# Kernel tuning notes

Hardware: AMD Instinct MI355X
Metric: run time of the kernel (lower is better)

## Reference

```python
import jax, jax.numpy as jnp
import numpy as np

B, T, C = 4, 2048, 1024
H = 16
D = C // H  # head_dim = 64


def setup_inputs() -> dict:
    key = jax.random.key(0)
    k1, k2, k3 = jax.random.split(key, 3)
    x = jax.random.normal(k1, (B, T, C), dtype=jnp.float32)
    w_qkv = jax.random.normal(k2, (3 * C, C), dtype=jnp.float32) * (1.0 / np.sqrt(C))
    w_proj = jax.random.normal(k3, (C, C), dtype=jnp.float32) * (1.0 / np.sqrt(C))
    return {"x": x, "w_qkv": w_qkv, "w_proj": w_proj}


def reference(x, w_qkv, w_proj):
    Bx, Tx, Cx = x.shape
    qkv = jnp.einsum('btc,fc->btf', x, w_qkv)  # [B,T,3C]
    q, k, v = jnp.split(qkv, 3, axis=-1)
    # [B,H,T,D]
    q = q.reshape(Bx, Tx, H, D).transpose(0, 2, 1, 3)
    k = k.reshape(Bx, Tx, H, D).transpose(0, 2, 1, 3)
    v = v.reshape(Bx, Tx, H, D).transpose(0, 2, 1, 3)
    scale = 1.0 / np.sqrt(D)
    scores = jnp.einsum('bhqd,bhkd->bhqk', q, k) * scale
    causal = jnp.tril(jnp.ones((Tx, Tx), dtype=bool))
    scores = jnp.where(causal, scores, jnp.finfo(scores.dtype).min)
    attn = jax.nn.softmax(scores, axis=-1)
    out = jnp.einsum('bhqk,bhkd->bhqd', attn, v)  # [B,H,T,D]
    out = out.transpose(0, 2, 1, 3).reshape(Bx, Tx, Cx)
    return jnp.einsum('btc,oc->bto', out, w_proj)
```

## Files before the change

### kernel.cpp

```cpp
#include <hip/hip_runtime.h>
#include <hip/hip_bf16.h>
#include <stdint.h>

#define Bx 4
#define Tx 2048
#define Cx 1024
#define Hx 16
#define Dx 64
#define Mx (Bx*Tx)

typedef __bf16 bf16x8 __attribute__((ext_vector_type(8)));
typedef float f32x4 __attribute__((ext_vector_type(4)));
typedef unsigned short u16x8 __attribute__((ext_vector_type(8)));

__device__ __forceinline__ unsigned short f2bf(float f) {
  union { float f; unsigned u; } v; v.f = f;
  unsigned r = v.u + 0x7fffu + ((v.u >> 16) & 1u);
  return (unsigned short)(r >> 16);
}

__global__ void cvt_kernel(const float* __restrict__ in, unsigned short* __restrict__ out, int n) {
  int i = blockIdx.x * blockDim.x + threadIdx.x;
  int idx = i << 3;
  if (idx >= n) return;
  const float4* p = (const float4*)(in + idx);
  float4 a = p[0], b = p[1];
  u16x8 o;
  o[0] = f2bf(a.x); o[1] = f2bf(a.y); o[2] = f2bf(a.z); o[3] = f2bf(a.w);
  o[4] = f2bf(b.x); o[5] = f2bf(b.y); o[6] = f2bf(b.z); o[7] = f2bf(b.w);
  *(u16x8*)(out + idx) = o;
}

#define GLOAD_LDS16(g, l) \
  __builtin_amdgcn_global_load_lds((const __attribute__((address_space(1))) void*)(g), \
                                   (__attribute__((address_space(3))) void*)(l), 16, 0, 0)

template<int OUT_F32>
__global__ __launch_bounds__(256) void gemm_nt(const unsigned short* __restrict__ A,
                                               const unsigned short* __restrict__ Bm,
                                               void* __restrict__ Cv,
                                               int M, int N, int K)
{
  __shared__ unsigned short As[128 * 32];
  __shared__ unsigned short Bs[128 * 32];
  const int tid  = threadIdx.x;
  const int wave = tid >> 6, lane = tid & 63;
  const int l15 = lane & 15, l4 = lane >> 4;
  const int mBase = blockIdx.y << 7;
  const int nBase = blockIdx.x << 7;
  const int wm = wave >> 1, wn = wave & 1;

  const int srow  = (wave << 4) + (lane >> 2);
  const int skcol = (lane & 3) << 3;

  f32x4 acc[4][4];
  #pragma unroll
  for (int i = 0; i < 4; ++i)
    #pragma unroll
    for (int j = 0; j < 4; ++j) { acc[i][j][0] = 0.f; acc[i][j][1] = 0.f; acc[i][j][2] = 0.f; acc[i][j][3] = 0.f; }

  const unsigned short* aRow = A  + (size_t)(mBase + srow) * K + skcol;
  const unsigned short* bRow = Bm + (size_t)(nBase + srow) * K + skcol;
  unsigned short* aL0 = As + (wave << 9);
  unsigned short* bL0 = Bs + (wave << 9);

  for (int k0 = 0; k0 < K; k0 += 32) {
    GLOAD_LDS16(aRow + k0,                   aL0);
    GLOAD_LDS16(aRow + (size_t)64 * K + k0,  aL0 + 2048);
    GLOAD_LDS16(bRow + k0,                   bL0);
    GLOAD_LDS16(bRow + (size_t)64 * K + k0,  bL0 + 2048);
    __syncthreads();

    bf16x8 af[4], bfr[4];
    #pragma unroll
    for (int mi = 0; mi < 4; ++mi)
      af[mi] = *(const bf16x8*)&As[((wm << 6) + (mi << 4) + l15) * 32 + (l4 << 3)];
    #pragma unroll
    for (int nj = 0; nj < 4; ++nj)
      bfr[nj] = *(const bf16x8*)&Bs[((wn << 6) + (nj << 4) + l15) * 32 + (l4 << 3)];
    #pragma unroll
    for (int mi = 0; mi < 4; ++mi)
      #pragma unroll
      for (int nj = 0; nj < 4; ++nj)
        acc[mi][nj] = __builtin_amdgcn_mfma_f32_16x16x32_bf16(af[mi], bfr[nj], acc[mi][nj], 0, 0, 0);
    __syncthreads();
  }

  #pragma unroll
  for (int mi = 0; mi < 4; ++mi) {
    #pragma unroll
    for (int nj = 0; nj < 4; ++nj) {
      const int row = mBase + (wm << 6) + (mi << 4) + (l4 << 2);
      const int col = nBase + (wn << 6) + (nj << 4) + l15;
      #pragma unroll
      for (int r = 0; r < 4; ++r) {
        float v = acc[mi][nj][r];
        if (OUT_F32) ((float*)Cv)[(size_t)(row + r) * N + col] = v;
        else ((unsigned short*)Cv)[(size_t)(row + r) * N + col] = f2bf(v);
      }
    }
  }
}

__global__ void vtrans_kernel(const unsigned short* __restrict__ qkv, unsigned short* __restrict__ vt) {
  const int bh = blockIdx.y;
  const int b = bh >> 4, h = bh & 15;
  const int t0 = blockIdx.x << 6;
  __shared__ unsigned short tile[64][65];
  const int tid = threadIdx.x;
  const unsigned short* src = qkv + (size_t)b * Tx * 3072 + 2048 + h * 64;
  for (int e = tid; e < 4096; e += 256) {
    int r = e >> 6, c = e & 63;
    tile[c][r] = src[(size_t)(t0 + r) * 3072 + c];
  }
  __syncthreads();
  unsigned short* dst = vt + (size_t)bh * 64 * Tx + t0;
  for (int e = tid; e < 4096; e += 256) {
    int d = e >> 6, tt = e & 63;
    dst[(size_t)d * Tx + tt] = tile[d][tt];
  }
}

__device__ __forceinline__ void compute_half(
    const unsigned short* __restrict__ Ks, const unsigned short* __restrict__ Vs,
    unsigned short* __restrict__ Plw,
    bf16x8 aq0, bf16x8 aq1, float* m_run, float* rs, f32x4* oacc,
    int qrow0, int kv0, bool diag, int l15, int l4)
{
  const float SC = 0.125f * 1.44269504f;
  f32x4 s[4];
  #pragma unroll
  for (int nt = 0; nt < 4; ++nt) { s[nt][0]=0.f; s[nt][1]=0.f; s[nt][2]=0.f; s[nt][3]=0.f; }
  #pragma unroll
  for (int nt = 0; nt < 4; ++nt) {
    const int r = (nt << 4) + l15, sz = r & 7;
    bf16x8 bk0 = *(const bf16x8*)&Ks[r * 64 + ((l4 ^ sz) << 3)];
    bf16x8 bk1 = *(const bf16x8*)&Ks[r * 64 + (((l4 + 4) ^ sz) << 3)];
    s[nt] = __builtin_amdgcn_mfma_f32_16x16x32_bf16(aq0, bk0, s[nt], 0, 0, 0);
    s[nt] = __builtin_amdgcn_mfma_f32_16x16x32_bf16(aq1, bk1, s[nt], 0, 0, 0);
  }
  #pragma unroll
  for (int nt = 0; nt < 4; ++nt) {
    const int kv = kv0 + (nt << 4) + l15;
    #pragma unroll
    for (int r = 0; r < 4; ++r) {
      float val = s[nt][r] * SC;
      if (diag && kv > qrow0 + (l4 << 2) + r) val = -3.0e38f;
      s[nt][r] = val;
    }
  }
  float pm[4];
  #pragma unroll
  for (int r = 0; r < 4; ++r)
    pm[r] = fmaxf(fmaxf(s[0][r], s[1][r]), fmaxf(s[2][r], s[3][r]));
  int ok = (pm[0] <= m_run[0] + 8.f) & (pm[1] <= m_run[1] + 8.f)
         & (pm[2] <= m_run[2] + 8.f) & (pm[3] <= m_run[3] + 8.f);
  if (!__all(ok)) {
    #pragma unroll
    for (int off = 1; off < 16; off <<= 1)
      #pragma unroll
      for (int r = 0; r < 4; ++r) pm[r] = fmaxf(pm[r], __shfl_xor(pm[r], off));
    #pragma unroll
    for (int r = 0; r < 4; ++r) {
      float mnew = fmaxf(m_run[r], pm[r]);
      float corr = exp2f(m_run[r] - mnew);
      rs[r] *= corr;
      #pragma unroll
      for (int nt = 0; nt < 4; ++nt) oacc[nt][r] *= corr;
      m_run[r] = mnew;
    }
  }
  #pragma unroll
  for (int nt = 0; nt < 4; ++nt)
    #pragma unroll
    for (int r = 0; r < 4; ++r) {
      float p = exp2f(s[nt][r] - m_run[r]);
      s[nt][r] = p;
      rs[r] += p;
    }
  #pragma unroll
  for (int nt = 0; nt < 4; ++nt)
    #pragma unroll
    for (int r = 0; r < 4; ++r)
      Plw[((l4 << 2) + r) * 72 + (nt << 4) + l15] = f2bf(s[nt][r]);
  asm volatile("s_waitcnt lgkmcnt(0)" ::: "memory");
  __builtin_amdgcn_sched_barrier(0);
  bf16x8 ap0 = *(const bf16x8*)&Plw[l15 * 72 + (l4 << 3)];
  bf16x8 ap1 = *(const bf16x8*)&Plw[l15 * 72 + 32 + (l4 << 3)];
  #pragma unroll
  for (int nt = 0; nt < 4; ++nt) {
    const int r = (nt << 4) + l15, vz = r & 7;
    bf16x8 bv0 = *(const bf16x8*)&Vs[r * 64 + ((l4 ^ vz) << 3)];
    bf16x8 bv1 = *(const bf16x8*)&Vs[r * 64 + (((l4 + 4) ^ vz) << 3)];
    oacc[nt] = __builtin_amdgcn_mfma_f32_16x16x32_bf16(ap0, bv0, oacc[nt], 0, 0, 0);
    oacc[nt] = __builtin_amdgcn_mfma_f32_16x16x32_bf16(ap1, bv1, oacc[nt], 0, 0, 0);
  }
}

__global__ __launch_bounds__(256, 4) void attn_kernel(const unsigned short* __restrict__ qkv,
                                                      const unsigned short* __restrict__ vt,
                                                      unsigned short* __restrict__ aout)
{
  const int id = blockIdx.x;
  const int xcd = id & 7, sblk = id >> 3;
  const int xblk = sblk & 15;
  const int bh = (xcd << 3) + (sblk >> 4);
  const int b = bh >> 4, h = bh & 15;
  const int wave = threadIdx.x >> 6, lane = threadIdx.x & 63;
  const int l15 = lane & 15, l4 = lane >> 4;
  const int qi0 = (xblk << 2) + wave;

  const unsigned short* qp = qkv + (size_t)b * Tx * 3072 + h * 64;
  const unsigned short* kp = qp + 1024;
  const unsigned short* vp = vt + (size_t)bh * 64 * Tx;
  unsigned short* op = aout + (size_t)b * Tx * 1024 + h * 64;

  __shared__ unsigned short Ks[64 * 64];
  __shared__ unsigned short Vs[64 * 64];
  __shared__ unsigned short Pl[4][2][16 * 72];

  const int qiA = qi0, qiB = 127 - qi0;
  const int qrA = qiA << 4, qrB = qiB << 4;
  const int lastA = xblk, lastB = 31 - xblk;

  bf16x8 aqA0 = *(const bf16x8*)&qp[(size_t)(qrA + l15) * 3072 + (l4 << 3)];
  bf16x8 aqA1 = *(const bf16x8*)&qp[(size_t)(qrA + l15) * 3072 + 32 + (l4 << 3)];
  bf16x8 aqB0 = *(const bf16x8*)&qp[(size_t)(qrB + l15) * 3072 + (l4 << 3)];
  bf16x8 aqB1 = *(const bf16x8*)&qp[(size_t)(qrB + l15) * 3072 + 32 + (l4 << 3)];

  float mA[4], rsA[4], mB[4], rsB[4];
  f32x4 oA[4], oB[4];
  #pragma unroll
  for (int r = 0; r < 4; ++r) { mA[r]=0.f; rsA[r]=0.f; mB[r]=0.f; rsB[r]=0.f; }
  #pragma unroll
  for (int nt = 0; nt < 4; ++nt) {
    oA[nt][0]=0.f; oA[nt][1]=0.f; oA[nt][2]=0.f; oA[nt][3]=0.f;
    oB[nt][0]=0.f; oB[nt][1]=0.f; oB[nt][2]=0.f; oB[nt][3]=0.f;
  }

  const int srw = lane >> 3;
  const int sj  = (lane & 7) ^ srw;

  for (int kvt = 0; kvt <= lastB; ++kvt) {
    const int kv0 = kvt << 6;
    {
      const int c0 = wave << 1, c1 = c0 + 1;
      const int r0 = (c0 << 3) + srw, r1 = (c1 << 3) + srw;
      GLOAD_LDS16(kp + (size_t)(kv0 + r0) * 3072 + (sj << 3), Ks + (c0 << 9));
      GLOAD_LDS16(kp + (size_t)(kv0 + r1) * 3072 + (sj << 3), Ks + (c1 << 9));
      GLOAD_LDS16(vp + (size_t)r0 * 2048 + kv0 + (sj << 3),   Vs + (c0 << 9));
      GLOAD_LDS16(vp + (size_t)r1 * 2048 + kv0 + (sj << 3),   Vs + (c1 << 9));
    }
    __syncthreads();

    compute_half(Ks, Vs, Pl[wave][1], aqB0, aqB1, mB, rsB, oB, qrB, kv0, kvt == lastB, l15, l4);
    if (kvt <= lastA)
      compute_half(Ks, Vs, Pl[wave][0], aqA0, aqA1, mA, rsA, oA, qrA, kv0, kvt == lastA, l15, l4);

    __syncthreads();
  }

  #pragma unroll
  for (int off = 1; off < 16; off <<= 1)
    #pragma unroll
    for (int r = 0; r < 4; ++r) { rsA[r] += __shfl_xor(rsA[r], off); rsB[r] += __shfl_xor(rsB[r], off); }
  #pragma unroll
  for (int r = 0; r < 4; ++r) {
    const float invA = 1.0f / rsA[r], invB = 1.0f / rsB[r];
    #pragma unroll
    for (int nt = 0; nt < 4; ++nt) {
      op[(size_t)(qrA + (l4 << 2) + r) * 1024 + (nt << 4) + l15] = f2bf(oA[nt][r] * invA);
      op[(size_t)(qrB + (l4 << 2) + r) * 1024 + (nt << 4) + l15] = f2bf(oB[nt][r] * invB);
    }
  }
}

extern "C" void kernel_launch(void* const* d_in, const int* in_sizes, int n_in,
                              void* d_out, int out_size, void* d_ws, size_t ws_size,
                              hipStream_t stream) {
  const float* x     = (const float*)d_in[0];
  const float* wqkv  = (const float*)d_in[1];
  const float* wproj = (const float*)d_in[2];

  char* ws = (char*)d_ws;
  unsigned short* qkvb = (unsigned short*)(ws);
  unsigned short* vtb  = (unsigned short*)(ws + 50331648);
  unsigned short* xb   = (unsigned short*)(ws + 50331648 + 16777216);
  unsigned short* wqb  = (unsigned short*)(ws + 50331648 + 16777216 + 16777216);
  unsigned short* wpb  = (unsigned short*)(ws + 50331648 + 16777216 + 16777216 + 6291456);
  unsigned short* aob  = xb;

  cvt_kernel<<<4096, 256, 0, stream>>>(x,     xb,  Bx * Tx * Cx);
  cvt_kernel<<<1536, 256, 0, stream>>>(wqkv,  wqb, 3 * Cx * Cx);
  cvt_kernel<<<512,  256, 0, stream>>>(wproj, wpb, Cx * Cx);

  gemm_nt<0><<<dim3(24, 64), 256, 0, stream>>>(xb, wqb, qkvb, Mx, 3072, 1024);
  vtrans_kernel<<<dim3(32, 64), 256, 0, stream>>>(qkvb, vtb);
  attn_kernel<<<1024, 256, 0, stream>>>(qkvb, vtb, aob);
  gemm_nt<1><<<dim3(8, 64), 256, 0, stream>>>(aob, wpb, d_out, Mx, 1024, 1024);
}
```

Measured before the change: 309.5 us.

## Rewrite bf16 GEMMs with double-buffered LDS, 256x128 tiles, swizzle and XCD remap

Replaces the single-buffered 128x128x32 GEMM with a 512-thread kernel using 256x128 tiles, K-step 64 and double-buffered direct-to-LDS loads. The next tile's loads are issued before computing on the current one, waiting only with vmcnt. LDS chunks are XOR-swizzled to reduce bank conflicts. Block IDs are remapped across the 8 XCDs for L2 locality, and MFMA sections get raised wave priority. The aim is to hide global-load latency and raise MFMA utilisation in the QKV and projection GEMMs, at the cost of more LDS per block and lower occupancy.

```diff
diff --git a/kernel.cpp b/kernel.cpp
--- a/kernel.cpp
+++ b/kernel.cpp
@@ -36,58 +36,87 @@
                                    (__attribute__((address_space(3))) void*)(l), 16, 0, 0)
 
 template<int OUT_F32>
-__global__ __launch_bounds__(256) void gemm_nt(const unsigned short* __restrict__ A,
-                                               const unsigned short* __restrict__ Bm,
-                                               void* __restrict__ Cv,
-                                               int M, int N, int K)
+__global__ __launch_bounds__(512, 1) void gemm8p(const unsigned short* __restrict__ A,
+                                                 const unsigned short* __restrict__ Bm,
+                                                 void* __restrict__ Cv,
+                                                 int M, int N, int K)
 {
-  __shared__ unsigned short As[128 * 32];
-  __shared__ unsigned short Bs[128 * 32];
-  const int tid  = threadIdx.x;
+  __shared__ unsigned short As[2][256 * 64];
+  __shared__ unsigned short Bs[2][128 * 64];
+  const int tid = threadIdx.x;
   const int wave = tid >> 6, lane = tid & 63;
   const int l15 = lane & 15, l4 = lane >> 4;
-  const int mBase = blockIdx.y << 7;
-  const int nBase = blockIdx.x << 7;
   const int wm = wave >> 1, wn = wave & 1;
-
-  const int srow  = (wave << 4) + (lane >> 2);
-  const int skcol = (lane & 3) << 3;
+  const int NB = N >> 7;
+  const int cpx = (int)gridDim.x >> 3;
+  const int bid = (int)blockIdx.x;
+  const int swz = (bid & 7) * cpx + (bid >> 3);
+  const int bx = swz % NB, by = swz / NB;
+  const int mBase = by << 8, nBase = bx << 7;
+
+  const int srow   = tid >> 3;
+  const int schunk = (tid & 7) ^ (srow & 7);
+  const unsigned short* aSrc = A  + (size_t)(mBase + srow) * K + (schunk << 3);
+  const unsigned short* bSrc = Bm + (size_t)(nBase + srow) * K + (schunk << 3);
+  const int dstOff = wave << 9;
 
   f32x4 acc[4][4];
   #pragma unroll
   for (int i = 0; i < 4; ++i)
     #pragma unroll
-    for (int j = 0; j < 4; ++j) { acc[i][j][0] = 0.f; acc[i][j][1] = 0.f; acc[i][j][2] = 0.f; acc[i][j][3] = 0.f; }
-
-  const unsigned short* aRow = A  + (size_t)(mBase + srow) * K + skcol;
-  const unsigned short* bRow = Bm + (size_t)(nBase + srow) * K + skcol;
-  unsigned short* aL0 = As + (wave << 9);
-  unsigned short* bL0 = Bs + (wave << 9);
-
-  for (int k0 = 0; k0 < K; k0 += 32) {
-    GLOAD_LDS16(aRow + k0,                   aL0);
-    GLOAD_LDS16(aRow + (size_t)64 * K + k0,  aL0 + 2048);
-    GLOAD_LDS16(bRow + k0,                   bL0);
-    GLOAD_LDS16(bRow + (size_t)64 * K + k0,  bL0 + 2048);
-    __syncthreads();
-
-    bf16x8 af[4], bfr[4];
-    #pragma unroll
-    for (int mi = 0; mi < 4; ++mi)
-      af[mi] = *(const bf16x8*)&As[((wm << 6) + (mi << 4) + l15) * 32 + (l4 << 3)];
-    #pragma unroll
-    for (int nj = 0; nj < 4; ++nj)
-      bfr[nj] = *(const bf16x8*)&Bs[((wn << 6) + (nj << 4) + l15) * 32 + (l4 << 3)];
-    #pragma unroll
-    for (int mi = 0; mi < 4; ++mi)
+    for (int j = 0; j < 4; ++j) { acc[i][j][0]=0.f; acc[i][j][1]=0.f; acc[i][j][2]=0.f; acc[i][j][3]=0.f; }
+
+  const int NT = K >> 6;
+  const int s7 = l15 & 7;
+
+#define STAGE6(k0, buf) do { \
+    GLOAD_LDS16(aSrc + (k0),                   &As[buf][dstOff]); \
+    GLOAD_LDS16(aSrc + (size_t) 64*K + (k0),   &As[buf][ 4096 + dstOff]); \
+    GLOAD_LDS16(aSrc + (size_t)128*K + (k0),   &As[buf][ 8192 + dstOff]); \
+    GLOAD_LDS16(aSrc + (size_t)192*K + (k0),   &As[buf][12288 + dstOff]); \
+    GLOAD_LDS16(bSrc + (k0),                   &Bs[buf][dstOff]); \
+    GLOAD_LDS16(bSrc + (size_t) 64*K + (k0),   &Bs[buf][ 4096 + dstOff]); \
+  } while (0)
+
+  STAGE6(0, 0);
+  for (int t = 0; t < NT; ++t) {
+    const int buf = t & 1;
+    if (t + 1 < NT) {
+      STAGE6((t + 1) << 6, buf ^ 1);
+      asm volatile("s_waitcnt vmcnt(6)" ::: "memory");
+    } else {
+      asm volatile("s_waitcnt vmcnt(0)" ::: "memory");
+    }
+    __builtin_amdgcn_s_barrier();
+    asm volatile("" ::: "memory");
+
+    const unsigned short* curA = As[buf];
+    const unsigned short* curB = Bs[buf];
+    #pragma unroll
+    for (int kk = 0; kk < 2; ++kk) {
+      const int ch = ((kk << 2) | l4) ^ s7;
+      bf16x8 af[4], bfr[4];
+      #pragma unroll
+      for (int mi = 0; mi < 4; ++mi)
+        af[mi]  = *(const bf16x8*)&curA[((wm << 6) + (mi << 4) + l15) * 64 + (ch << 3)];
       #pragma unroll
       for (int nj = 0; nj < 4; ++nj)
-        acc[mi][nj] = __builtin_amdgcn_mfma_f32_16x16x32_bf16(af[mi], bfr[nj], acc[mi][nj], 0, 0, 0);
-    __syncthreads();
-  }
-
-  #pragma unroll
-  for (int mi = 0; mi < 4; ++mi) {
+        bfr[nj] = *(const bf16x8*)&curB[((wn << 6) + (nj << 4) + l15) * 64 + (ch << 3)];
+      __builtin_amdgcn_s_setprio(1);
+      #pragma unroll
+      for (int mi = 0; mi < 4; ++mi)
+        #pragma unroll
+        for (int nj = 0; nj < 4; ++nj)
+          acc[mi][nj] = __builtin_amdgcn_mfma_f32_16x16x32_bf16(af[mi], bfr[nj], acc[mi][nj], 0, 0, 0);
+      __builtin_amdgcn_s_setprio(0);
+    }
+    asm volatile("" ::: "memory");
+    __builtin_amdgcn_s_barrier();
+  }
+#undef STAGE6
+
+  #pragma unroll
+  for (int mi = 0; mi < 4; ++mi)
     #pragma unroll
     for (int nj = 0; nj < 4; ++nj) {
       const int row = mBase + (wm << 6) + (mi << 4) + (l4 << 2);
@@ -99,7 +128,6 @@
         else ((unsigned short*)Cv)[(size_t)(row + r) * N + col] = f2bf(v);
       }
     }
-  }
 }
 
 __global__ void vtrans_kernel(const unsigned short* __restrict__ qkv, unsigned short* __restrict__ vt) {
@@ -294,8 +322,8 @@
   cvt_kernel<<<1536, 256, 0, stream>>>(wqkv,  wqb, 3 * Cx * Cx);
   cvt_kernel<<<512,  256, 0, stream>>>(wproj, wpb, Cx * Cx);
 
-  gemm_nt<0><<<dim3(24, 64), 256, 0, stream>>>(xb, wqb, qkvb, Mx, 3072, 1024);
+  gemm8p<0><<<dim3(768), 512, 0, stream>>>(xb, wqb, qkvb, Mx, 3072, 1024);
   vtrans_kernel<<<dim3(32, 64), 256, 0, stream>>>(qkvb, vtb);
   attn_kernel<<<1024, 256, 0, stream>>>(qkvb, vtb, aob);
-  gemm_nt<1><<<dim3(8, 64), 256, 0, stream>>>(aob, wpb, d_out, Mx, 1024, 1024);
-}
+  gemm8p<1><<<dim3(256), 512, 0, stream>>>(aob, wpb, d_out, Mx, 1024, 1024);
+}
```

Measured after the change: 298.9 us. 1.04x faster.
